# Performance work log

Measured on AMD Instinct MI355X. Metric: run time of the kernel, lower is better.

The kernel has to match this reference:

```python
import jax, jax.numpy as jnp
import numpy as np

HIDDEN = 256
B = 1024
T = 1024
IN_DIM = 2
OUT_DIM = 2
DECAY = 0.8  # integrator decay per step


def setup_inputs() -> dict:
    key = jax.random.key(0)
    k_x, k_win, k_bin, k_wout, k_bout, k_tau = jax.random.split(key, 6)
    x_seq = jax.random.normal(k_x, (B, T, IN_DIM), dtype=jnp.float32)
    # nn.Linear init: U(-1/sqrt(fan_in), 1/sqrt(fan_in))
    lim_in = 1.0 / np.sqrt(IN_DIM)
    lim_out = 1.0 / np.sqrt(HIDDEN)
    W_in = jax.random.uniform(k_win, (HIDDEN, IN_DIM), jnp.float32, -lim_in, lim_in)
    b_in = jax.random.uniform(k_bin, (HIDDEN,), jnp.float32, -lim_in, lim_in)
    W_out = jax.random.uniform(k_wout, (OUT_DIM, HIDDEN), jnp.float32, -lim_out, lim_out)
    b_out = jax.random.uniform(k_bout, (OUT_DIM,), jnp.float32, -lim_out, lim_out)
    tau_m = jax.random.uniform(k_tau, (HIDDEN,), jnp.float32, 0.0, 4.0)
    return {"x_seq": x_seq, "W_in": W_in, "b_in": b_in,
            "W_out": W_out, "b_out": b_out, "tau_m": tau_m}


def reference(x_seq, W_in, b_in, W_out, b_out, tau_m):
    # Precompute input currents for all timesteps with one big GEMM: [B,T,H]
    currents = jnp.einsum('bti,hi->bth', x_seq, W_in) + b_in
    alpha = jax.nn.sigmoid(tau_m)  # [H], constant across time

    v0 = jnp.zeros((x_seq.shape[0], W_in.shape[0]), dtype=x_seq.dtype)
    integ0 = jnp.zeros((x_seq.shape[0], W_out.shape[0]), dtype=x_seq.dtype)

    def step(carry, cur_t):
        v, integ = carry
        v = v * alpha + (1.0 - alpha) * cur_t          # LIF membrane update
        spikes = (v >= 1.0).astype(v.dtype)            # hard threshold
        v = v - spikes                                 # soft reset
        out_current = spikes @ W_out.T + b_out         # [B, 2]
        integ = DECAY * integ + out_current
        return (v, integ), None

    # scan over time axis: currents transposed to [T, B, H]
    (v_f, integ_f), _ = jax.lax.scan(step, (v0, integ0),
                                     jnp.swapaxes(currents, 0, 1))
    return integ_f
```

## Files before the change

### kernel.cpp

```cpp
#include <hip/hip_runtime.h>
#include <math.h>


constexpr int T_STEPS = 1024;
constexpr int HIDDEN  = 256;
constexpr int BLK     = 128;
constexpr int NENT    = T_STEPS / 2;

typedef float f32x2 __attribute__((ext_vector_type(2)));
typedef float f32x4 __attribute__((ext_vector_type(4)));

static __device__ __forceinline__ f32x2 pk_mul(f32x2 a, f32x2 b) {
    f32x2 d; asm("v_pk_mul_f32 %0, %1, %2" : "=v"(d) : "v"(a), "v"(b)); return d;
}
static __device__ __forceinline__ f32x2 pk_add(f32x2 a, f32x2 b) {
    f32x2 d; asm("v_pk_add_f32 %0, %1, %2" : "=v"(d) : "v"(a), "v"(b)); return d;
}
static __device__ __forceinline__ f32x2 pk_fma(f32x2 a, f32x2 b, f32x2 c) {
    f32x2 d; asm("v_pk_fma_f32 %0, %1, %2, %3" : "=v"(d) : "v"(a), "v"(b), "v"(c)); return d;
}
static __device__ __forceinline__ f32x2 pk_mul_bc0(f32x2 x, f32x2 w) {
    f32x2 d; asm("v_pk_mul_f32 %0, %1, %2 op_sel:[0,0] op_sel_hi:[0,1]"
                 : "=v"(d) : "v"(x), "v"(w)); return d;
}
static __device__ __forceinline__ f32x2 pk_mul_bc1(f32x2 x, f32x2 w) {
    f32x2 d; asm("v_pk_mul_f32 %0, %1, %2 op_sel:[1,0] op_sel_hi:[1,1]"
                 : "=v"(d) : "v"(x), "v"(w)); return d;
}
static __device__ __forceinline__ float spike_neg(float v) {
    return __builtin_amdgcn_fmed3f(-floorf(v), -1.0f, 0.0f);
}

__global__ __launch_bounds__(BLK) void sfnn_med3_kernel(
    const float* __restrict__ x_seq,
    const float* __restrict__ W_in,
    const float* __restrict__ b_in,
    const float* __restrict__ W_out,
    const float* __restrict__ b_out,
    const float* __restrict__ tau_m,
    float* __restrict__ out)
{
    __shared__ f32x4 xs[NENT];
    __shared__ float red[4];

    const int b   = blockIdx.x;
    const int tid = threadIdx.x;
    const int h0  = tid;
    const int h1  = tid + BLK;

    const f32x4* __restrict__ xg =
        reinterpret_cast<const f32x4*>(x_seq) + (size_t)b * NENT;
    #pragma unroll
    for (int k = 0; k < NENT / BLK; ++k)
        xs[tid + k * BLK] = xg[tid + k * BLK];

    f32x2 w0p, w1p, bip, alp, bep, c08;
    w0p.x = W_in[2 * h0];     w0p.y = W_in[2 * h1];
    w1p.x = W_in[2 * h0 + 1]; w1p.y = W_in[2 * h1 + 1];
    bip.x = b_in[h0];         bip.y = b_in[h1];
    alp.x = 1.0f / (1.0f + expf(-tau_m[h0]));
    alp.y = 1.0f / (1.0f + expf(-tau_m[h1]));
    bep.x = 1.0f - alp.x;     bep.y = 1.0f - alp.y;
    c08.x = 0.8f;             c08.y = 0.8f;

    __syncthreads();

    f32x2 v  = {0.0f, 0.0f};
    f32x2 Sn = {0.0f, 0.0f};

    #define LIF_STEP(XP)                                                      \
        {                                                                     \
            f32x2 cur = pk_add(pk_add(pk_mul_bc0((XP), w0p),                  \
                                      pk_mul_bc1((XP), w1p)), bip);           \
            v = pk_add(pk_mul(v, alp), pk_mul(bep, cur));                     \
            f32x2 spn;                                                        \
            spn.x = spike_neg(v.x);                                           \
            spn.y = spike_neg(v.y);                                           \
            v  = pk_add(v, spn);                                              \
            Sn = pk_fma(c08, Sn, spn);                                        \
        }
    #define LIF2(Q)                                                           \
        LIF_STEP(__builtin_shufflevector((Q), (Q), 0, 1))                     \
        LIF_STEP(__builtin_shufflevector((Q), (Q), 2, 3))

    f32x4 q0 = xs[0];
    f32x4 q1 = xs[1];
    f32x4 q2 = xs[2];
    f32x4 q3 = xs[3];
    for (int i = 0; i < NENT - 4; i += 4) {
        LIF2(q0) q0 = xs[i + 4];
        LIF2(q1) q1 = xs[i + 5];
        LIF2(q2) q2 = xs[i + 6];
        LIF2(q3) q3 = xs[i + 7];
    }
    LIF2(q0) LIF2(q1) LIF2(q2) LIF2(q3)
    #undef LIF2
    #undef LIF_STEP

    const float Sx = -Sn.x, Sy = -Sn.y;
    float r0 = fmaf(Sy, W_out[h1],          Sx * W_out[h0]);
    float r1 = fmaf(Sy, W_out[HIDDEN + h1], Sx * W_out[HIDDEN + h0]);
    #pragma unroll
    for (int off = 32; off > 0; off >>= 1) {
        r0 += __shfl_xor(r0, off, 64);
        r1 += __shfl_xor(r1, off, 64);
    }
    const int wave = tid >> 6;
    if ((tid & 63) == 0) {
        red[2 * wave]     = r0;
        red[2 * wave + 1] = r1;
    }
    __syncthreads();
    if (tid == 0) {
        const float geo = 5.0f;
        out[2 * b]     = (red[0] + red[2]) + b_out[0] * geo;
        out[2 * b + 1] = (red[1] + red[3]) + b_out[1] * geo;
    }
}

extern "C" void kernel_launch(void* const* d_in, const int* in_sizes, int n_in,
                              void* d_out, int out_size, void* d_ws, size_t ws_size,
                              hipStream_t stream) {
    const float* x_seq = (const float*)d_in[0];
    const float* W_in  = (const float*)d_in[1];
    const float* b_in  = (const float*)d_in[2];
    const float* W_out = (const float*)d_in[3];
    const float* b_out = (const float*)d_in[4];
    const float* tau_m = (const float*)d_in[5];
    float* out = (float*)d_out;

    sfnn_med3_kernel<<<dim3(1024), dim3(BLK), 0, stream>>>(
        x_seq, W_in, b_in, W_out, b_out, tau_m, out);
}
```

Before: 59.41 us.

## Use one wave per batch row with four hidden units per thread

Shrinks each block to a single 64-thread wavefront, with each thread now running four hidden neurons as two packed pairs instead of two. The per-step LDS read of x is shared across more neurons, and the cross-wave shared-memory reduction and its second barrier go away. The cost is half as many threads per batch row and a longer serial chain per thread. Whether occupancy and latency hiding stay adequate with 1024 single-wave blocks on the device is the open question.

```diff
diff --git a/kernel.cpp b/kernel.cpp
--- a/kernel.cpp
+++ b/kernel.cpp
@@ -4,7 +4,7 @@
 
 constexpr int T_STEPS = 1024;
 constexpr int HIDDEN  = 256;
-constexpr int BLK     = 128;
+constexpr int BLK     = 64;
 constexpr int NENT    = T_STEPS / 2;
 
 typedef float f32x2 __attribute__((ext_vector_type(2)));
@@ -31,7 +31,7 @@
     return __builtin_amdgcn_fmed3f(-floorf(v), -1.0f, 0.0f);
 }
 
-__global__ __launch_bounds__(BLK) void sfnn_med3_kernel(
+__global__ __launch_bounds__(BLK) void sfnn_w1_kernel(
     const float* __restrict__ x_seq,
     const float* __restrict__ W_in,
     const float* __restrict__ b_in,
@@ -41,12 +41,11 @@
     float* __restrict__ out)
 {
     __shared__ f32x4 xs[NENT];
-    __shared__ float red[4];
 
     const int b   = blockIdx.x;
     const int tid = threadIdx.x;
-    const int h0  = tid;
-    const int h1  = tid + BLK;
+    const int hA0 = tid,       hA1 = tid + 64;
+    const int hB0 = tid + 128, hB1 = tid + 192;
 
     const f32x4* __restrict__ xg =
         reinterpret_cast<const f32x4*>(x_seq) + (size_t)b * NENT;
@@ -54,30 +53,40 @@
     for (int k = 0; k < NENT / BLK; ++k)
         xs[tid + k * BLK] = xg[tid + k * BLK];
 
-    f32x2 w0p, w1p, bip, alp, bep, c08;
-    w0p.x = W_in[2 * h0];     w0p.y = W_in[2 * h1];
-    w1p.x = W_in[2 * h0 + 1]; w1p.y = W_in[2 * h1 + 1];
-    bip.x = b_in[h0];         bip.y = b_in[h1];
-    alp.x = 1.0f / (1.0f + expf(-tau_m[h0]));
-    alp.y = 1.0f / (1.0f + expf(-tau_m[h1]));
-    bep.x = 1.0f - alp.x;     bep.y = 1.0f - alp.y;
-    c08.x = 0.8f;             c08.y = 0.8f;
+    f32x2 w0A, w1A, biA, alA, beA, w0B, w1B, biB, alB, beB, c08;
+    w0A.x = W_in[2*hA0];   w0A.y = W_in[2*hA1];
+    w1A.x = W_in[2*hA0+1]; w1A.y = W_in[2*hA1+1];
+    biA.x = b_in[hA0];     biA.y = b_in[hA1];
+    w0B.x = W_in[2*hB0];   w0B.y = W_in[2*hB1];
+    w1B.x = W_in[2*hB0+1]; w1B.y = W_in[2*hB1+1];
+    biB.x = b_in[hB0];     biB.y = b_in[hB1];
+    alA.x = 1.0f / (1.0f + expf(-tau_m[hA0]));
+    alA.y = 1.0f / (1.0f + expf(-tau_m[hA1]));
+    alB.x = 1.0f / (1.0f + expf(-tau_m[hB0]));
+    alB.y = 1.0f / (1.0f + expf(-tau_m[hB1]));
+    beA.x = 1.0f - alA.x;  beA.y = 1.0f - alA.y;
+    beB.x = 1.0f - alB.x;  beB.y = 1.0f - alB.y;
+    c08.x = 0.8f;          c08.y = 0.8f;
 
     __syncthreads();
 
-    f32x2 v  = {0.0f, 0.0f};
-    f32x2 Sn = {0.0f, 0.0f};
+    f32x2 vA  = {0.0f, 0.0f}, vB  = {0.0f, 0.0f};
+    f32x2 SnA = {0.0f, 0.0f}, SnB = {0.0f, 0.0f};
 
     #define LIF_STEP(XP)                                                      \
         {                                                                     \
-            f32x2 cur = pk_add(pk_add(pk_mul_bc0((XP), w0p),                  \
-                                      pk_mul_bc1((XP), w1p)), bip);           \
-            v = pk_add(pk_mul(v, alp), pk_mul(bep, cur));                     \
-            f32x2 spn;                                                        \
-            spn.x = spike_neg(v.x);                                           \
-            spn.y = spike_neg(v.y);                                           \
-            v  = pk_add(v, spn);                                              \
-            Sn = pk_fma(c08, Sn, spn);                                        \
+            f32x2 curA = pk_add(pk_add(pk_mul_bc0((XP), w0A),                 \
+                                       pk_mul_bc1((XP), w1A)), biA);          \
+            f32x2 curB = pk_add(pk_add(pk_mul_bc0((XP), w0B),                 \
+                                       pk_mul_bc1((XP), w1B)), biB);          \
+            vA = pk_add(pk_mul(vA, alA), pk_mul(beA, curA));                  \
+            vB = pk_add(pk_mul(vB, alB), pk_mul(beB, curB));                  \
+            f32x2 spA, spB;                                                   \
+            spA.x = spike_neg(vA.x);  spA.y = spike_neg(vA.y);                \
+            spB.x = spike_neg(vB.x);  spB.y = spike_neg(vB.y);                \
+            vA = pk_add(vA, spA);     vB = pk_add(vB, spB);                   \
+            SnA = pk_fma(c08, SnA, spA);                                      \
+            SnB = pk_fma(c08, SnB, spB);                                      \
         }
     #define LIF2(Q)                                                           \
         LIF_STEP(__builtin_shufflevector((Q), (Q), 0, 1))                     \
@@ -97,24 +106,20 @@
     #undef LIF2
     #undef LIF_STEP
 
-    const float Sx = -Sn.x, Sy = -Sn.y;
-    float r0 = fmaf(Sy, W_out[h1],          Sx * W_out[h0]);
-    float r1 = fmaf(Sy, W_out[HIDDEN + h1], Sx * W_out[HIDDEN + h0]);
+    const float SAx = -SnA.x, SAy = -SnA.y, SBx = -SnB.x, SBy = -SnB.y;
+    const float* __restrict__ Wo0 = W_out;
+    const float* __restrict__ Wo1 = W_out + HIDDEN;
+    float r0 = SAx * Wo0[hA0] + SAy * Wo0[hA1] + SBx * Wo0[hB0] + SBy * Wo0[hB1];
+    float r1 = SAx * Wo1[hA0] + SAy * Wo1[hA1] + SBx * Wo1[hB0] + SBy * Wo1[hB1];
     #pragma unroll
     for (int off = 32; off > 0; off >>= 1) {
         r0 += __shfl_xor(r0, off, 64);
         r1 += __shfl_xor(r1, off, 64);
     }
-    const int wave = tid >> 6;
-    if ((tid & 63) == 0) {
-        red[2 * wave]     = r0;
-        red[2 * wave + 1] = r1;
-    }
-    __syncthreads();
     if (tid == 0) {
         const float geo = 5.0f;
-        out[2 * b]     = (red[0] + red[2]) + b_out[0] * geo;
-        out[2 * b + 1] = (red[1] + red[3]) + b_out[1] * geo;
+        out[2 * b]     = r0 + b_out[0] * geo;
+        out[2 * b + 1] = r1 + b_out[1] * geo;
     }
 }
 
@@ -129,6 +134,6 @@
     const float* tau_m = (const float*)d_in[5];
     float* out = (float*)d_out;
 
-    sfnn_med3_kernel<<<dim3(1024), dim3(BLK), 0, stream>>>(
+    sfnn_w1_kernel<<<dim3(1024), dim3(BLK), 0, stream>>>(
         x_seq, W_in, b_in, W_out, b_out, tau_m, out);
 }
```

Result: slower. 63.11 us (+6.2%).
